# Kernel optimization log

Hardware: AMD Instinct MI355X
Metric: run time of the kernel (lower is better)

## Reference

```python
import jax, jax.numpy as jnp
import numpy as np

B, E, H, SEQ = 4096, 512, 512, 128


def setup_inputs() -> dict:
    key = jax.random.key(0)
    ks = jax.random.split(key, 7)
    s = 1.0 / np.sqrt(H)  # PyTorch LSTM init scale
    return {
        "start_emb": jax.random.normal(ks[0], (B, 1, E), dtype=jnp.float32),
        "h0": jax.random.normal(ks[1], (1, B, H), dtype=jnp.float32),
        "c0": jax.random.normal(ks[2], (1, B, H), dtype=jnp.float32),
        "w_ih": jax.random.normal(ks[3], (4 * H, E), dtype=jnp.float32) * s,
        "w_hh": jax.random.normal(ks[4], (4 * H, H), dtype=jnp.float32) * s,
        "b_ih": jax.random.normal(ks[5], (4 * H,), dtype=jnp.float32) * s,
        "b_hh": jax.random.normal(ks[6], (4 * H,), dtype=jnp.float32) * s,
        "seq_length": SEQ,
    }


def reference(start_emb, h0, c0, w_ih, w_hh, b_ih, b_hh, seq_length):
    # start_emb: [B, 1, E] -- identical input every step, so precompute its projection once.
    x = start_emb[:, 0, :]                       # [B, E]
    x_proj = x @ w_ih.T + b_ih + b_hh            # [B, 4H], constant across steps
    hdim = w_hh.shape[1]

    def step(carry, _):
        h, c = carry                              # each [B, H]
        gates = x_proj + h @ w_hh.T               # [B, 4H]
        i, f, g, o = jnp.split(gates, 4, axis=-1) # PyTorch gate order i,f,g,o
        i = jax.nn.sigmoid(i)
        f = jax.nn.sigmoid(f)
        g = jnp.tanh(g)
        o = jax.nn.sigmoid(o)
        c = f * c + i * g
        h = o * jnp.tanh(c)
        return (h, c), None

    (h, c), _ = jax.lax.scan(step, (h0[0], c0[0]), None, length=seq_length)
    # Return final (h_n, c_n) with the [num_layers=1, B, H] leading dim, as PyTorch does.
    return h[None], c[None]
```

## Files before the change

### kernel.cpp

```cpp
#include <hip/hip_runtime.h>
#include <hip/hip_bf16.h>

#define BATCH 4096
#define KD    512
#define NG    2048
#define SEQLEN 128

typedef __attribute__((ext_vector_type(8))) short short8;
typedef __attribute__((ext_vector_type(4))) float floatx4;

#define HWREG_XCC_ID (20 | (0 << 6) | ((4 - 1) << 11))

__device__ __forceinline__ void gld16(const void* g, void* l) {
  __builtin_amdgcn_global_load_lds(
      (const __attribute__((address_space(1))) void*)g,
      (__attribute__((address_space(3))) void*)l, 16, 0, 0);
}

__device__ __forceinline__ float fast_sig(float x) {
  return __builtin_amdgcn_rcpf(1.0f + __expf(-x));
}
__device__ __forceinline__ float fast_tanh(float x) {
  return 1.0f - 2.0f * __builtin_amdgcn_rcpf(1.0f + __expf(2.0f * x));
}

__device__ __forceinline__ unsigned pack_bf16(float lo, float hi) {
  unsigned ul = (unsigned)__builtin_bit_cast(unsigned short, __float2bfloat16(lo));
  unsigned uh = (unsigned)__builtin_bit_cast(unsigned short, __float2bfloat16(hi));
  return (uh << 16) | ul;
}
__device__ __forceinline__ float unpack_lo(unsigned u) {
  u <<= 16; return __builtin_bit_cast(float, u);
}
__device__ __forceinline__ float unpack_hi(unsigned u) {
  u &= 0xffff0000u; return __builtin_bit_cast(float, u);
}

template <int TBM, int TBN, int NT>
__device__ __forceinline__ void gemm_tile(const short* __restrict__ A,
                                          const short* __restrict__ Bw,
                                          floatx4 acc[4][4],
                                          short* lA, short* lB,
                                          int bm, int bn,
                                          int lane, int wm, int wn, int tid) {
#pragma unroll 1
  for (int kt = 0; kt < KD / 64; ++kt) {
    const int k0 = kt * 64;
#pragma unroll
    for (int i = 0; i < TBM * 8 / NT; ++i) {
      int q = i * NT + tid;
      int row = q >> 3, cs = q & 7;
      int cc = cs ^ (row & 7);
      gld16(A + (size_t)(bm + row) * KD + k0 + cc * 8, lA + q * 8);
    }
#pragma unroll
    for (int i = 0; i < TBN * 8 / NT; ++i) {
      int q = i * NT + tid;
      int row = q >> 3, cs = q & 7;
      int cc = cs ^ (row & 7);
      gld16(Bw + (size_t)(bn + row) * KD + k0 + cc * 8, lB + q * 8);
    }
    __syncthreads();
#pragma unroll
    for (int ks = 0; ks < 2; ++ks) {
      short8 a[4], b[4];
#pragma unroll
      for (int mi = 0; mi < 4; ++mi) {
        int arow = wm * 64 + mi * 16 + (lane & 15);
        int ch = (ks * 4 + (lane >> 4)) ^ (arow & 7);
        a[mi] = *(const short8*)&lA[arow * 64 + ch * 8];
      }
#pragma unroll
      for (int j = 0; j < 4; ++j) {
        int brow = wn * 64 + j * 16 + (lane & 15);
        int ch = (ks * 4 + (lane >> 4)) ^ (brow & 7);
        b[j] = *(const short8*)&lB[brow * 64 + ch * 8];
      }
#pragma unroll
      for (int mi = 0; mi < 4; ++mi)
#pragma unroll
        for (int j = 0; j < 4; ++j)
          acc[mi][j] =
              __builtin_amdgcn_mfma_f32_16x16x32_bf16(a[mi], b[j], acc[mi][j], 0, 0, 0);
    }
    __syncthreads();
  }
}

__device__ __forceinline__ void group_barrier_xcd(unsigned* cnt, unsigned target) {
  __syncthreads();
  if (threadIdx.x == 0) {
    __hip_atomic_fetch_add(cnt, 1u, __ATOMIC_RELAXED, __HIP_MEMORY_SCOPE_AGENT);
    while (__hip_atomic_load(cnt, __ATOMIC_RELAXED, __HIP_MEMORY_SCOPE_AGENT) <
           target) {
      __builtin_amdgcn_s_sleep(1);
    }
    asm volatile("buffer_inv sc0" ::: "memory");
    asm volatile("s_waitcnt vmcnt(0)" ::: "memory");
  }
  __syncthreads();
}

__global__ __launch_bounds__(512, 1) void lstm_persist(
    const short* __restrict__ xbf,
    const short* __restrict__ wih,
    const short* __restrict__ whh,
    const float* __restrict__ biasp,
    const float* __restrict__ c0,
    short* __restrict__ hA, short* __restrict__ hB,
    float* __restrict__ outH, float* __restrict__ outC,
    unsigned* __restrict__ sync_area) {
  __shared__ __align__(16) short lA[128 * 64];
  __shared__ __align__(16) short lB[256 * 64];

  const int tid = threadIdx.x;
  const int lane = tid & 63;
  const int wid = tid >> 6;
  const int wm = wid >> 2;
  const int wn = wid & 3;

  __shared__ int sh_bx, sh_by;
  if (tid == 0) {
    int px = __builtin_amdgcn_s_getreg(HWREG_XCC_ID) & 7;
    unsigned r = __hip_atomic_fetch_add(&sync_area[px], 1u, __ATOMIC_RELAXED,
                                        __HIP_MEMORY_SCOPE_AGENT);
    sh_bx = px * 4 + (int)(r >> 3);
    sh_by = (int)(r & 7);
  }
  __syncthreads();
  const int bx = sh_bx, by = sh_by;
  const int bm = bx * 128;
  const int bn = by * 256;
  unsigned* gcnt = sync_area + 256 + bx * 32;

  const int houter = by * 4 + wn;
  const int hcol = houter * 16 + (lane & 15);
  const int rb = houter * 64 + (lane & 15);

  floatx4 acc[4][4] = {};
  gemm_tile<128, 256, 512>(xbf, wih, acc, lA, lB, bm, bn, lane, wm, wn, tid);

  const float b0 = biasp[rb], b1 = biasp[rb + 16], b2 = biasp[rb + 32],
              b3 = biasp[rb + 48];
  unsigned xprP[4][4][2];
  float creg[4][4];
#pragma unroll
  for (int mi = 0; mi < 4; ++mi) {
    const int mrow0 = bm + wm * 64 + mi * 16 + (lane >> 4) * 4;
#pragma unroll
    for (int reg = 0; reg < 4; ++reg) {
      xprP[mi][reg][0] = pack_bf16(acc[mi][0][reg] + b0, acc[mi][1][reg] + b1);
      xprP[mi][reg][1] = pack_bf16(acc[mi][2][reg] + b2, acc[mi][3][reg] + b3);
      creg[mi][reg] = c0[(size_t)(mrow0 + reg) * KD + hcol];
    }
  }

#pragma unroll 1
  for (int t = 0; t < SEQLEN; ++t) {
    const short* hin = (t & 1) ? hB : hA;
    short* hout = (t & 1) ? hA : hB;

#pragma unroll
    for (int mi = 0; mi < 4; ++mi)
#pragma unroll
      for (int j = 0; j < 4; ++j)
        acc[mi][j] = floatx4{0.f, 0.f, 0.f, 0.f};

    gemm_tile<128, 256, 512>(hin, whh, acc, lA, lB, bm, bn, lane, wm, wn, tid);

#pragma unroll
    for (int mi = 0; mi < 4; ++mi) {
      const int mrow0 = bm + wm * 64 + mi * 16 + (lane >> 4) * 4;
#pragma unroll
      for (int reg = 0; reg < 4; ++reg) {
        const int m = mrow0 + reg;
        float gi = acc[mi][0][reg] + unpack_lo(xprP[mi][reg][0]);
        float gf = acc[mi][1][reg] + unpack_hi(xprP[mi][reg][0]);
        float gg = acc[mi][2][reg] + unpack_lo(xprP[mi][reg][1]);
        float go = acc[mi][3][reg] + unpack_hi(xprP[mi][reg][1]);
        float si = fast_sig(gi);
        float sf = fast_sig(gf);
        float tg = fast_tanh(gg);
        float so = fast_sig(go);
        float cn = sf * creg[mi][reg] + si * tg;
        creg[mi][reg] = cn;
        float hn = so * fast_tanh(cn);
        const size_t ci = (size_t)m * KD + hcol;
        ((__hip_bfloat16*)hout)[ci] = __float2bfloat16(hn);
        if (t == SEQLEN - 1) {
          outH[ci] = hn;
          outC[ci] = cn;
        }
      }
    }
    if (t != SEQLEN - 1) group_barrier_xcd(gcnt, 8u * (unsigned)(t + 1));
  }
}

__global__ __launch_bounds__(256, 2) void lstm_step(
    const short* __restrict__ hin, __hip_bfloat16* __restrict__ hout_bf,
    const short* __restrict__ W, const float* __restrict__ xp,
    float* __restrict__ c, float* __restrict__ hout_f32) {
  __shared__ __align__(16) short lA[128 * 64];
  __shared__ __align__(16) short lB[128 * 64];
  const int tid = threadIdx.x;
  const int lane = tid & 63;
  const int wid = tid >> 6;
  const int wm = wid >> 1, wn = wid & 1;
  const int bm = blockIdx.x * 128, bn = blockIdx.y * 128;

  floatx4 acc[4][4] = {};
  gemm_tile<128, 128, 256>(hin, W, acc, lA, lB, bm, bn, lane, wm, wn, tid);

  const int houter = blockIdx.y * 2 + wn;
  const int hcol = houter * 16 + (lane & 15);
  const int rb = houter * 64 + (lane & 15);
#pragma unroll
  for (int mi = 0; mi < 4; ++mi) {
    const int mrow0 = bm + wm * 64 + mi * 16 + (lane >> 4) * 4;
#pragma unroll
    for (int reg = 0; reg < 4; ++reg) {
      const int m = mrow0 + reg;
      const float* xpr = xp + (size_t)m * NG + rb;
      float si = fast_sig(acc[mi][0][reg] + xpr[0]);
      float sf = fast_sig(acc[mi][1][reg] + xpr[16]);
      float tg = fast_tanh(acc[mi][2][reg] + xpr[32]);
      float so = fast_sig(acc[mi][3][reg] + xpr[48]);
      const int ci = m * KD + hcol;
      float cn = sf * c[ci] + si * tg;
      c[ci] = cn;
      float hn = so * fast_tanh(cn);
      hout_bf[ci] = __float2bfloat16(hn);
      if (hout_f32) hout_f32[ci] = hn;
    }
  }
}

__global__ __launch_bounds__(256, 2) void xproj_gemm(
    const short* __restrict__ xbf, const short* __restrict__ Wih,
    const float* __restrict__ biasp, float* __restrict__ xp) {
  __shared__ __align__(16) short lA[128 * 64];
  __shared__ __align__(16) short lB[128 * 64];
  const int tid = threadIdx.x;
  const int lane = tid & 63;
  const int wid = tid >> 6;
  const int wm = wid >> 1, wn = wid & 1;
  const int bm = blockIdx.x * 128, bn = blockIdx.y * 128;

  floatx4 acc[4][4] = {};
  gemm_tile<128, 128, 256>(xbf, Wih, acc, lA, lB, bm, bn, lane, wm, wn, tid);

  const int houter = blockIdx.y * 2 + wn;
  const int rb = houter * 64 + (lane & 15);
  const float b0 = biasp[rb], b1 = biasp[rb + 16], b2 = biasp[rb + 32],
              b3 = biasp[rb + 48];
#pragma unroll
  for (int mi = 0; mi < 4; ++mi) {
    const int mrow0 = bm + wm * 64 + mi * 16 + (lane >> 4) * 4;
#pragma unroll
    for (int reg = 0; reg < 4; ++reg) {
      float* xpr = xp + (size_t)(mrow0 + reg) * NG + rb;
      xpr[0]  = acc[mi][0][reg] + b0;
      xpr[16] = acc[mi][1][reg] + b1;
      xpr[32] = acc[mi][2][reg] + b2;
      xpr[48] = acc[mi][3][reg] + b3;
    }
  }
}

__global__ void permw_k(const float* __restrict__ w,
                        __hip_bfloat16* __restrict__ o) {
  int idx = blockIdx.x * 256 + threadIdx.x;
  int r = idx >> 9, k = idx & 511;
  int hout = r >> 6, g = (r >> 4) & 3, hin = r & 15;
  o[idx] = __float2bfloat16(w[(size_t)((g << 9) + hout * 16 + hin) * 512 + k]);
}

__global__ void bias_k(const float* __restrict__ bi, const float* __restrict__ bh,
                       float* __restrict__ o) {
  int r = blockIdx.x * 256 + threadIdx.x;
  int hout = r >> 6, g = (r >> 4) & 3, hin = r & 15;
  int n = (g << 9) + hout * 16 + hin;
  o[r] = bi[n] + bh[n];
}

__global__ void f2bf_k(const float* __restrict__ in,
                       __hip_bfloat16* __restrict__ out, int n) {
  int i = blockIdx.x * 256 + threadIdx.x;
  if (i < n) out[i] = __float2bfloat16(in[i]);
}

extern "C" void kernel_launch(void* const* d_in, const int* in_sizes, int n_in,
                              void* d_out, int out_size, void* d_ws, size_t ws_size,
                              hipStream_t stream) {
  const float* start_emb = (const float*)d_in[0];
  const float* h0 = (const float*)d_in[1];
  const float* c0 = (const float*)d_in[2];
  const float* w_ih = (const float*)d_in[3];
  const float* w_hh = (const float*)d_in[4];
  const float* b_ih = (const float*)d_in[5];
  const float* b_hh = (const float*)d_in[6];

  char* ws = (char*)d_ws;
  __hip_bfloat16* whh_p = (__hip_bfloat16*)(ws);
  __hip_bfloat16* wih_p = (__hip_bfloat16*)(ws + (2ll << 20));
  __hip_bfloat16* xbf   = (__hip_bfloat16*)(ws + (4ll << 20));
  __hip_bfloat16* hbufA = (__hip_bfloat16*)(ws + (8ll << 20));
  __hip_bfloat16* hbufB = (__hip_bfloat16*)(ws + (12ll << 20));
  float* biasp          = (float*)(ws + (16ll << 20));
  unsigned* sync_area   = (unsigned*)(ws + (16ll << 20) + 65536);
  float* xp             = (float*)(ws + (17ll << 20));

  float* outH = (float*)d_out;
  float* outC = (float*)d_out + (size_t)BATCH * KD;

  permw_k<<<4096, 256, 0, stream>>>(w_hh, whh_p);
  permw_k<<<4096, 256, 0, stream>>>(w_ih, wih_p);
  bias_k<<<8, 256, 0, stream>>>(b_ih, b_hh, biasp);
  f2bf_k<<<8192, 256, 0, stream>>>(start_emb, xbf, BATCH * KD);
  f2bf_k<<<8192, 256, 0, stream>>>(h0, hbufA, BATCH * KD);
  (void)hipMemsetAsync(sync_area, 0, 8192, stream);

  const short* a_xbf = (const short*)xbf;
  const short* a_wih = (const short*)wih_p;
  const short* a_whh = (const short*)whh_p;
  const float* a_bias = biasp;
  const float* a_c0 = c0;
  short* a_hA = (short*)hbufA;
  short* a_hB = (short*)hbufB;
  float* a_outH = outH;
  float* a_outC = outC;
  unsigned* a_sync = sync_area;
  void* args[] = {&a_xbf, &a_wih, &a_whh, &a_bias, &a_c0,
                  &a_hA, &a_hB, &a_outH, &a_outC, &a_sync};
  hipError_t e = hipLaunchCooperativeKernel((const void*)lstm_persist,
                                            dim3(256), dim3(512), args,
                                            34 * 1024, stream);
  if (e != hipSuccess) {
    (void)hipMemcpyAsync(outC, c0, (size_t)BATCH * KD * sizeof(float),
                         hipMemcpyDeviceToDevice, stream);
    dim3 grid(BATCH / 128, NG / 128);
    xproj_gemm<<<grid, 256, 0, stream>>>((const short*)xbf, (const short*)wih_p,
                                         biasp, xp);
    for (int t = 0; t < SEQLEN; ++t) {
      const short* hin = (const short*)((t & 1) ? hbufB : hbufA);
      __hip_bfloat16* hout = (t & 1) ? hbufA : hbufB;
      lstm_step<<<grid, 256, 0, stream>>>(hin, hout, (const short*)whh_p, xp,
                                          outC, (t == SEQLEN - 1) ? outH : nullptr);
    }
  }
}
```

Measured before the change: 1.630 ms.

## Double-buffer LDS k-tiles in persistent LSTM GEMM and prefetch next-step weights

Replaces the single-buffered gemm_tile with a two-stage LDS pipeline. Each k-tile's A and B slices are loaded asynchronously while the MFMAs run on the previous tile. During the last k-iteration it also preloads the first W_hh tile for the next timestep, so that load can overlap the epilogue and the grid barrier. Static LDS roughly doubles and the dynamic shared-memory request is dropped. Correctness now depends on the async global-to-LDS loads being complete before each barrier.

```diff
diff --git a/kernel.cpp b/kernel.cpp
--- a/kernel.cpp
+++ b/kernel.cpp
@@ -34,6 +34,49 @@
 }
 __device__ __forceinline__ float unpack_hi(unsigned u) {
   u &= 0xffff0000u; return __builtin_bit_cast(float, u);
+}
+
+template <int NCH>
+__device__ __forceinline__ void stage_tile(const short* __restrict__ src,
+                                           int base_row, int k0,
+                                           short* __restrict__ dst, int tid) {
+#pragma unroll
+  for (int i = 0; i < NCH; ++i) {
+    int q = i * 512 + tid;
+    int row = q >> 3;
+    int cc = (q & 7) ^ (row & 7);
+    gld16(src + (size_t)(base_row + row) * KD + k0 + cc * 8, dst + q * 8);
+  }
+}
+
+__device__ __forceinline__ void compute_tile(const short* __restrict__ a_lds,
+                                             const short* __restrict__ b_lds,
+                                             floatx4 acc[4][4], int lane,
+                                             int wm, int wn) {
+#pragma unroll
+  for (int ks = 0; ks < 2; ++ks) {
+    short8 a[4], b[4];
+#pragma unroll
+    for (int mi = 0; mi < 4; ++mi) {
+      int arow = wm * 64 + mi * 16 + (lane & 15);
+      int ch = (ks * 4 + (lane >> 4)) ^ (arow & 7);
+      a[mi] = *(const short8*)&a_lds[arow * 64 + ch * 8];
+    }
+#pragma unroll
+    for (int j = 0; j < 4; ++j) {
+      int brow = wn * 64 + j * 16 + (lane & 15);
+      int ch = (ks * 4 + (lane >> 4)) ^ (brow & 7);
+      b[j] = *(const short8*)&b_lds[brow * 64 + ch * 8];
+    }
+    __builtin_amdgcn_s_setprio(1);
+#pragma unroll
+    for (int mi = 0; mi < 4; ++mi)
+#pragma unroll
+      for (int j = 0; j < 4; ++j)
+        acc[mi][j] =
+            __builtin_amdgcn_mfma_f32_16x16x32_bf16(a[mi], b[j], acc[mi][j], 0, 0, 0);
+    __builtin_amdgcn_s_setprio(0);
+  }
 }
 
 template <int TBM, int TBN, int NT>
@@ -110,8 +153,8 @@
     short* __restrict__ hA, short* __restrict__ hB,
     float* __restrict__ outH, float* __restrict__ outC,
     unsigned* __restrict__ sync_area) {
-  __shared__ __align__(16) short lA[128 * 64];
-  __shared__ __align__(16) short lB[256 * 64];
+  __shared__ __align__(16) short lA[2][128 * 64];
+  __shared__ __align__(16) short lB[2][256 * 64];
 
   const int tid = threadIdx.x;
   const int lane = tid & 63;
@@ -138,7 +181,20 @@
   const int rb = houter * 64 + (lane & 15);
 
   floatx4 acc[4][4] = {};
-  gemm_tile<128, 256, 512>(xbf, wih, acc, lA, lB, bm, bn, lane, wm, wn, tid);
+  stage_tile<2>(xbf, bm, 0, lA[0], tid);
+  stage_tile<4>(wih, bn, 0, lB[0], tid);
+  __syncthreads();
+#pragma unroll 2
+  for (int kt = 0; kt < 8; ++kt) {
+    if (kt < 7) {
+      stage_tile<2>(xbf, bm, (kt + 1) * 64, lA[(kt + 1) & 1], tid);
+      stage_tile<4>(wih, bn, (kt + 1) * 64, lB[(kt + 1) & 1], tid);
+    } else {
+      stage_tile<4>(whh, bn, 0, lB[0], tid);
+    }
+    compute_tile(lA[kt & 1], lB[kt & 1], acc, lane, wm, wn);
+    __syncthreads();
+  }
 
   const float b0 = biasp[rb], b1 = biasp[rb + 16], b2 = biasp[rb + 32],
               b3 = biasp[rb + 48];
@@ -166,7 +222,19 @@
       for (int j = 0; j < 4; ++j)
         acc[mi][j] = floatx4{0.f, 0.f, 0.f, 0.f};
 
-    gemm_tile<128, 256, 512>(hin, whh, acc, lA, lB, bm, bn, lane, wm, wn, tid);
+    stage_tile<2>(hin, bm, 0, lA[0], tid);
+    __syncthreads();
+#pragma unroll 2
+    for (int kt = 0; kt < 8; ++kt) {
+      if (kt < 7) {
+        stage_tile<2>(hin, bm, (kt + 1) * 64, lA[(kt + 1) & 1], tid);
+        stage_tile<4>(whh, bn, (kt + 1) * 64, lB[(kt + 1) & 1], tid);
+      } else if (t < SEQLEN - 1) {
+        stage_tile<4>(whh, bn, 0, lB[0], tid);
+      }
+      compute_tile(lA[kt & 1], lB[kt & 1], acc, lane, wm, wn);
+      __syncthreads();
+    }
 
 #pragma unroll
     for (int mi = 0; mi < 4; ++mi) {
@@ -335,7 +403,7 @@
                   &a_hA, &a_hB, &a_outH, &a_outC, &a_sync};
   hipError_t e = hipLaunchCooperativeKernel((const void*)lstm_persist,
                                             dim3(256), dim3(512), args,
-                                            34 * 1024, stream);
+                                            0, stream);
   if (e != hipSuccess) {
     (void)hipMemcpyAsync(outC, c0, (size_t)BATCH * KD * sizeof(float),
                          hipMemcpyDeviceToDevice, stream);
```

After: 2.689 ms. +65.0%, slower.
